# Optimization experiments

Hardware: AMD Instinct MI355X
Metric: run time of the kernel (lower is better)

Reference implementation:

```python
import jax, jax.numpy as jnp
import numpy as np

B, L, E, H = 4, 2048, 1024, 16
HD = E // H  # head_dim = 64


def setup_inputs() -> dict:
    key = jax.random.key(0)
    ks = jax.random.split(key, 11)
    s = 1.0 / np.sqrt(E)
    return {
        "q": jax.random.normal(ks[0], (B, L, E), jnp.float32),
        "k": jax.random.normal(ks[1], (B, L, E), jnp.float32),
        "v": jax.random.normal(ks[2], (B, L, E), jnp.float32),
        "Wq": jax.random.normal(ks[3], (E, E), jnp.float32) * s,
        "bq": jax.random.normal(ks[4], (E,), jnp.float32) * s,
        "Wk": jax.random.normal(ks[5], (E, E), jnp.float32) * s,
        "bk": jax.random.normal(ks[6], (E,), jnp.float32) * s,
        "Wv": jax.random.normal(ks[7], (E, E), jnp.float32) * s,
        "bv": jax.random.normal(ks[8], (E,), jnp.float32) * s,
        "Wo": jax.random.normal(ks[9], (E, E), jnp.float32) * s,
        "bo": jax.random.normal(ks[10], (E,), jnp.float32) * s,
    }


def reference(q, k, v, Wq, bq, Wk, bk, Wv, bv, Wo, bo):
    # Linear projections (torch Linear: x @ W.T + b)
    qp = q @ Wq.T + bq  # [B, L, E]
    kp = k @ Wk.T + bk
    vp = v @ Wv.T + bv
    # split heads -> [B, H, L, HD]
    qh = qp.reshape(B, L, H, HD).transpose(0, 2, 1, 3)
    kh = kp.reshape(B, L, H, HD).transpose(0, 2, 1, 3)
    vh = vp.reshape(B, L, H, HD).transpose(0, 2, 1, 3)
    scale = 1.0 / jnp.sqrt(jnp.asarray(HD, qh.dtype))
    score = jnp.einsum("bhqd,bhkd->bhqk", qh, kh) * scale  # [B, H, L, L]
    attn = jax.nn.softmax(score, axis=-1)
    # dropout p=0 (eval) -> identity
    out = jnp.einsum("bhqk,bhkd->bhqd", attn, vh)  # [B, H, L, HD]
    out = out.transpose(0, 2, 1, 3).reshape(B, L, E)
    out = out @ Wo.T + bo
    # original returns attn flattened over (B*H); match that shape
    return out, attn.reshape(B * H, L, L)
```

## Files before the change

kernel.cpp:

```cpp
#include <hip/hip_runtime.h>
#include <stdint.h>

typedef __attribute__((ext_vector_type(8))) short bf16x8;
typedef __attribute__((ext_vector_type(4))) float f32x4;

#define DEV __device__ __forceinline__

static constexpr int Bsz = 4, Lsz = 2048, Esz = 1024, Hsz = 16, HDsz = 64;
static constexpr int BL = Bsz * Lsz;
static constexpr size_t PLANE = (size_t)BL * Esz;

DEV unsigned short f2bf(float x) {
  union { float f; unsigned u; } c; c.f = x;
  unsigned u = c.u + 0x7FFFu + ((c.u >> 16) & 1u);
  return (unsigned short)(u >> 16);
}
DEV float bf2f(unsigned short h) {
  union { unsigned u; float f; } c; c.u = ((unsigned)h) << 16; return c.f;
}
DEV bf16x8 ld_bf8(const unsigned short* p) { return *(const bf16x8*)p; }

template<bool A_F32, bool OUT_F32>
DEV void gemm_body(const void* __restrict__ Aptr, const float* __restrict__ W,
                   const float* __restrict__ bias, void* __restrict__ Cptr,
                   unsigned short (*As)[40], unsigned short (*Bs)[40])
{
  constexpr int Kdim = Esz, Ndim = Esz;
  const int t = threadIdx.x;
  const int lane = t & 63, wave = t >> 6;
  const int wr = wave >> 1, wc = wave & 1;
  const int frow = lane & 15, fg = lane >> 4;

  const int f = blockIdx.x + 8 * blockIdx.y;
  const int m_t = ((f & 7) << 3) + (f >> 6);
  const int n_t = (f >> 3) & 7;
  const int m0 = m_t * 128, n0 = n_t * 128;

  f32x4 acc[4][4];
#pragma unroll
  for (int i = 0; i < 4; i++)
#pragma unroll
    for (int j = 0; j < 4; j++) acc[i][j] = f32x4{0.f, 0.f, 0.f, 0.f};

  for (int k0 = 0; k0 < Kdim; k0 += 32) {
    __syncthreads();
#pragma unroll
    for (int j = 0; j < 4; j++) {
      int s = t + j * 256, row = s >> 3, c4 = s & 7;
      if constexpr (A_F32) {
        const float* A = (const float*)Aptr;
        float4 v = *(const float4*)&A[(size_t)(m0 + row) * Kdim + k0 + c4 * 4];
        ushort4 hi;
        hi.x = f2bf(v.x); hi.y = f2bf(v.y); hi.z = f2bf(v.z); hi.w = f2bf(v.w);
        *(ushort4*)&As[row][c4 * 4] = hi;
      } else {
        const unsigned short* A = (const unsigned short*)Aptr;
        *(ushort4*)&As[row][c4 * 4] =
            *(const ushort4*)&A[(size_t)(m0 + row) * Kdim + k0 + c4 * 4];
      }
      {
        float4 v = *(const float4*)&W[(size_t)(n0 + row) * Kdim + k0 + c4 * 4];
        ushort4 hi;
        hi.x = f2bf(v.x); hi.y = f2bf(v.y); hi.z = f2bf(v.z); hi.w = f2bf(v.w);
        *(ushort4*)&Bs[row][c4 * 4] = hi;
      }
    }
    __syncthreads();

    bf16x8 ah[4], bhv[4];
#pragma unroll
    for (int x = 0; x < 4; x++) {
      ah[x] = ld_bf8(&As[wr * 64 + x * 16 + frow][fg * 8]);
      bhv[x] = ld_bf8(&Bs[wc * 64 + x * 16 + frow][fg * 8]);
    }
#pragma unroll
    for (int mi = 0; mi < 4; mi++)
#pragma unroll
      for (int ni = 0; ni < 4; ni++)
        acc[mi][ni] = __builtin_amdgcn_mfma_f32_16x16x32_bf16(ah[mi], bhv[ni], acc[mi][ni], 0, 0, 0);
  }

#pragma unroll
  for (int mi = 0; mi < 4; mi++)
#pragma unroll
    for (int ni = 0; ni < 4; ni++) {
      int col = n0 + wc * 64 + ni * 16 + frow;
      float bv = bias[col];
#pragma unroll
      for (int r = 0; r < 4; r++) {
        int row = m0 + wr * 64 + mi * 16 + fg * 4 + r;
        float val = acc[mi][ni][r] + bv;
        size_t idx = (size_t)row * Ndim + col;
        if constexpr (OUT_F32)
          __builtin_nontemporal_store(val, &((float*)Cptr)[idx]);
        else
          ((unsigned short*)Cptr)[idx] = f2bf(val);
      }
    }
}

__global__ __launch_bounds__(256) void gemm_proj3(
    const float* qA, const float* kA, const float* vA,
    const float* Wq, const float* Wk, const float* Wv,
    const float* bq, const float* bk, const float* bv,
    unsigned short* qC, unsigned short* kC, unsigned short* vC)
{
  __shared__ unsigned short As[128][40];
  __shared__ unsigned short Bs[128][40];
  const int z = blockIdx.z;
  const float* A = z == 0 ? qA : (z == 1 ? kA : vA);
  const float* W = z == 0 ? Wq : (z == 1 ? Wk : Wv);
  const float* bias = z == 0 ? bq : (z == 1 ? bk : bv);
  unsigned short* C = z == 0 ? qC : (z == 1 ? kC : vC);
  gemm_body<true, false>(A, W, bias, C, As, Bs);
}

__global__ __launch_bounds__(256) void gemm_out(
    const unsigned short* A, const float* W, const float* bias, float* C)
{
  __shared__ unsigned short As[128][40];
  __shared__ unsigned short Bs[128][40];
  gemm_body<false, true>(A, W, bias, C, As, Bs);
}

__global__ __launch_bounds__(256) void attn_fused(
    const unsigned short* __restrict__ qph, const unsigned short* __restrict__ kph,
    const unsigned short* __restrict__ vp,
    float* __restrict__ attn, unsigned short* __restrict__ oh)
{
  __shared__ unsigned short QP[64][72];
  __shared__ unsigned short Kh[64][72];
  __shared__ unsigned short Vt[64][72];

  const int t = threadIdx.x, lane = t & 63, wave = t >> 6;
  const int frow = lane & 15, fg = lane >> 4;

  const int f = blockIdx.x + 32 * blockIdx.y;
  const int bh = ((f & 7) << 3) + (f >> 8);
  const int qt = (f >> 3) & 31;
  const int b = bh >> 4, h = bh & 15;
  const int q0 = qt * 64;
  const int qw = q0 + wave * 16;

  const size_t base = (size_t)b * Lsz * Esz + (size_t)h * HDsz;
  constexpr float SC2 = 0.1803368801f;

  const int srow = t >> 4, sc4 = (t & 15) * 4;
  const int vrow = t >> 4, vc = t & 15;

  auto loadKh = [&](ushort4* r, int row0) {
#pragma unroll
    for (int j = 0; j < 4; j++)
      r[j] = *(const ushort4*)&kph[base + (size_t)(row0 + srow + j * 16) * Esz + sc4];
  };
  auto writeK = [&](unsigned short (*dst)[72], const ushort4* r) {
#pragma unroll
    for (int j = 0; j < 4; j++)
      *(ushort4*)&dst[srow + j * 16][sc4] = r[j];
  };
  auto loadV = [&](unsigned short (*rv)[4], int row0) {
#pragma unroll
    for (int j = 0; j < 4; j++) {
      size_t g = base + (size_t)(row0 + vrow + j * 16) * Esz + vc;
#pragma unroll
      for (int i = 0; i < 4; i++) rv[j][i] = vp[g + i * 16];
    }
  };
  auto writeV = [&](unsigned short (*rv)[4]) {
#pragma unroll
    for (int j = 0; j < 4; j++) {
#pragma unroll
      for (int i = 0; i < 4; i++) Vt[vc + i * 16][vrow + j * 16] = rv[j][i];
    }
  };

#pragma unroll
  for (int j = 0; j < 4; j++) {
    size_t g = base + (size_t)(q0 + srow + j * 16) * Esz + sc4;
    *(ushort4*)&QP[srow + j * 16][sc4] = *(const ushort4*)&qph[g];
  }
  __syncthreads();
  bf16x8 qfh[2];
#pragma unroll
  for (int dh = 0; dh < 2; dh++)
    qfh[dh] = ld_bf8(&QP[wave * 16 + frow][dh * 32 + fg * 8]);

  float zl[4];
#pragma unroll
  for (int r = 0; r < 4; r++) zl[r] = 0.f;

  auto computeA = [&](unsigned short (*Kc)[72]) {
#pragma unroll
    for (int kc = 0; kc < 4; kc++) {
      f32x4 sv = f32x4{0.f, 0.f, 0.f, 0.f};
#pragma unroll
      for (int dh = 0; dh < 2; dh++) {
        bf16x8 kf = ld_bf8(&Kc[kc * 16 + frow][dh * 32 + fg * 8]);
        sv = __builtin_amdgcn_mfma_f32_16x16x32_bf16(qfh[dh], kf, sv, 0, 0, 0);
      }
#pragma unroll
      for (int r = 0; r < 4; r++) zl[r] += exp2f(sv[r] * SC2);
    }
  };

  {
    ushort4 rA[4], rB[4];
    loadKh(rA, 0);
    loadKh(rB, 64);
    for (int kt = 0; kt < 32; kt += 2) {
      __syncthreads();
      writeK(Kh, rA);
      writeK(Vt, rB);
      if (kt + 2 < 32) {
        loadKh(rA, (kt + 2) * 64);
        loadKh(rB, (kt + 3) * 64);
      }
      __syncthreads();
      computeA(Kh);
      computeA(Vt);
    }
  }
  float rz[4];
#pragma unroll
  for (int r = 0; r < 4; r++) {
    float z = zl[r];
#pragma unroll
    for (int o = 1; o < 16; o <<= 1) z += __shfl_xor(z, o);
    rz[r] = 1.f / z;
  }

  f32x4 oacc[4];
#pragma unroll
  for (int d = 0; d < 4; d++) oacc[d] = f32x4{0.f, 0.f, 0.f, 0.f};

  const size_t arow = (size_t)bh * Lsz * Lsz;

  auto computeB = [&](int kt) {
    f32x4 sv[4];
#pragma unroll
    for (int kc = 0; kc < 4; kc++) {
      sv[kc] = f32x4{0.f, 0.f, 0.f, 0.f};
#pragma unroll
      for (int dh = 0; dh < 2; dh++) {
        bf16x8 kfh = ld_bf8(&Kh[kc * 16 + frow][dh * 32 + fg * 8]);
        sv[kc] = __builtin_amdgcn_mfma_f32_16x16x32_bf16(qfh[dh], kfh, sv[kc], 0, 0, 0);
      }
    }
#pragma unroll
    for (int kc = 0; kc < 4; kc++) {
#pragma unroll
      for (int r = 0; r < 4; r++) {
        float p = exp2f(sv[kc][r] * SC2) * rz[r];
        QP[wave * 16 + fg * 4 + r][kc * 16 + frow] = f2bf(p);
      }
    }
    __syncthreads();
#pragma unroll
    for (int it = 0; it < 4; it++) {
      int prow = it * 4 + fg;
      int pc = frow * 4;
      ushort4 pv4 = *(const ushort4*)&QP[wave * 16 + prow][pc];
      f32x4 w;
      w[0] = bf2f(pv4.x); w[1] = bf2f(pv4.y); w[2] = bf2f(pv4.z); w[3] = bf2f(pv4.w);
      __builtin_nontemporal_store(w,
          (f32x4*)&attn[arow + (size_t)(qw + prow) * Lsz + kt * 64 + pc]);
    }
#pragma unroll
    for (int kh2 = 0; kh2 < 2; kh2++) {
      bf16x8 pa = ld_bf8(&QP[wave * 16 + frow][kh2 * 32 + fg * 8]);
#pragma unroll
      for (int d = 0; d < 4; d++) {
        bf16x8 vb = ld_bf8(&Vt[d * 16 + frow][kh2 * 32 + fg * 8]);
        oacc[d] = __builtin_amdgcn_mfma_f32_16x16x32_bf16(pa, vb, oacc[d], 0, 0, 0);
      }
    }
  };

  {
    ushort4 khA[4], khB[4];
    unsigned short vA[4][4], vB[4][4];
    loadKh(khA, 0);
    loadV(vA, 0);
    for (int kt = 0; kt < 32; kt += 2) {
      __syncthreads();
      writeK(Kh, khA);
      writeV(vA);
      if (kt + 1 < 32) {
        loadKh(khB, (kt + 1) * 64);
        loadV(vB, (kt + 1) * 64);
      }
      __syncthreads();
      computeB(kt);
      __syncthreads();
      writeK(Kh, khB);
      writeV(vB);
      if (kt + 2 < 32) {
        loadKh(khA, (kt + 2) * 64);
        loadV(vA, (kt + 2) * 64);
      }
      __syncthreads();
      computeB(kt + 1);
    }
  }

#pragma unroll
  for (int d = 0; d < 4; d++)
#pragma unroll
    for (int r = 0; r < 4; r++) {
      int qrow = qw + fg * 4 + r;
      __builtin_nontemporal_store(f2bf(oacc[d][r]),
          &oh[base + (size_t)qrow * Esz + d * 16 + frow]);
    }
}

extern "C" void kernel_launch(void* const* d_in, const int* in_sizes, int n_in,
                              void* d_out, int out_size, void* d_ws, size_t ws_size,
                              hipStream_t stream)
{
  (void)in_sizes; (void)n_in; (void)out_size; (void)ws_size;

  const float* q  = (const float*)d_in[0];
  const float* k  = (const float*)d_in[1];
  const float* v  = (const float*)d_in[2];
  const float* Wq = (const float*)d_in[3];
  const float* bq = (const float*)d_in[4];
  const float* Wk = (const float*)d_in[5];
  const float* bk = (const float*)d_in[6];
  const float* Wv = (const float*)d_in[7];
  const float* bv = (const float*)d_in[8];
  const float* Wo = (const float*)d_in[9];
  const float* bo = (const float*)d_in[10];

  float* out  = (float*)d_out;
  float* attn = out + PLANE;

  unsigned short* qph = (unsigned short*)d_ws;
  unsigned short* kph = qph + PLANE;
  unsigned short* vpp = kph + PLANE;
  unsigned short* oh  = vpp + PLANE;

  dim3 bb(256);
  gemm_proj3<<<dim3(8, 64, 3), bb, 0, stream>>>(q, k, v, Wq, Wk, Wv,
                                                bq, bk, bv, qph, kph, vpp);

  dim3 ga(32, 64);
  attn_fused<<<ga, bb, 0, stream>>>(qph, kph, vpp, attn, oh);

  gemm_out<<<dim3(8, 64), bb, 0, stream>>>(oh, Wo, bo, out);
}
```

Baseline: 463.5 us.

## Move softmax denominator pass into separate kernel with larger 128x128 tiles

The first pass of the two-pass softmax, which sums exp of the scores per row, moves out of the fused attention kernel into a new zcalc kernel. zcalc uses 128-row Q tiles against 128-row K tiles so each K load is reused over twice as many query rows. It writes the reciprocal row sums to workspace, and attn_fused reads them instead of recomputing. A __syncthreads between writing P to shared memory and reading it back is also dropped. That removal looks safe only because each wave touches just its own 16 rows of QP, so it is a correctness risk if that ever changes.

```diff
diff --git a/kernel.cpp b/kernel.cpp
--- a/kernel.cpp
+++ b/kernel.cpp
@@ -123,9 +123,104 @@
   gemm_body<false, true>(A, W, bias, C, As, Bs);
 }
 
+__global__ __launch_bounds__(256) void zcalc(
+    const unsigned short* __restrict__ qph, const unsigned short* __restrict__ kph,
+    float* __restrict__ rzg)
+{
+  __shared__ unsigned short Qs[128][72];
+  __shared__ unsigned short Ks[128][72];
+
+  const int t = threadIdx.x, lane = t & 63, wave = t >> 6;
+  const int frow = lane & 15, fg = lane >> 4;
+
+  const int f = blockIdx.x + 16 * blockIdx.y;
+  const int bh = ((f & 7) << 3) + (f >> 7);
+  const int qt = (f >> 3) & 15;
+  const int b = bh >> 4, h = bh & 15;
+  const int q0 = qt * 128;
+  const size_t base = (size_t)b * Lsz * Esz + (size_t)h * HDsz;
+  constexpr float SC2 = 0.1803368801f;
+
+  const int srow = t >> 4, sc4 = (t & 15) * 4;
+
+  auto load128 = [&](ushort4* r, const unsigned short* src, int row0) {
+#pragma unroll
+    for (int j = 0; j < 8; j++)
+      r[j] = *(const ushort4*)&src[base + (size_t)(row0 + srow + j * 16) * Esz + sc4];
+  };
+  auto write128 = [&](unsigned short (*dst)[72], const ushort4* r) {
+#pragma unroll
+    for (int j = 0; j < 8; j++)
+      *(ushort4*)&dst[srow + j * 16][sc4] = r[j];
+  };
+
+  {
+    ushort4 rq[8];
+    load128(rq, qph, q0);
+    write128(Qs, rq);
+  }
+  __syncthreads();
+  bf16x8 qf[2][2];
+#pragma unroll
+  for (int mi = 0; mi < 2; mi++)
+#pragma unroll
+    for (int dh = 0; dh < 2; dh++)
+      qf[mi][dh] = ld_bf8(&Qs[wave * 32 + mi * 16 + frow][dh * 32 + fg * 8]);
+
+  float zl[2][4];
+#pragma unroll
+  for (int mi = 0; mi < 2; mi++)
+#pragma unroll
+    for (int r = 0; r < 4; r++) zl[mi][r] = 0.f;
+
+  auto compute = [&]() {
+#pragma unroll
+    for (int kf = 0; kf < 8; kf++) {
+      bf16x8 k0 = ld_bf8(&Ks[kf * 16 + frow][fg * 8]);
+      bf16x8 k1 = ld_bf8(&Ks[kf * 16 + frow][32 + fg * 8]);
+#pragma unroll
+      for (int mi = 0; mi < 2; mi++) {
+        f32x4 sv = f32x4{0.f, 0.f, 0.f, 0.f};
+        sv = __builtin_amdgcn_mfma_f32_16x16x32_bf16(qf[mi][0], k0, sv, 0, 0, 0);
+        sv = __builtin_amdgcn_mfma_f32_16x16x32_bf16(qf[mi][1], k1, sv, 0, 0, 0);
+#pragma unroll
+        for (int r = 0; r < 4; r++) zl[mi][r] += exp2f(sv[r] * SC2);
+      }
+    }
+  };
+
+  {
+    ushort4 rA[8], rB[8];
+    load128(rA, kph, 0);
+    for (int kt = 0; kt < 16; kt += 2) {
+      __syncthreads();
+      write128(Ks, rA);
+      if (kt + 1 < 16) load128(rB, kph, (kt + 1) * 128);
+      __syncthreads();
+      compute();
+      __syncthreads();
+      write128(Ks, rB);
+      if (kt + 2 < 16) load128(rA, kph, (kt + 2) * 128);
+      __syncthreads();
+      compute();
+    }
+  }
+
+#pragma unroll
+  for (int mi = 0; mi < 2; mi++)
+#pragma unroll
+    for (int r = 0; r < 4; r++) {
+      float z = zl[mi][r];
+#pragma unroll
+      for (int o = 1; o < 16; o <<= 1) z += __shfl_xor(z, o);
+      if (frow == 0)
+        rzg[(size_t)bh * Lsz + q0 + wave * 32 + mi * 16 + fg * 4 + r] = 1.f / z;
+    }
+}
+
 __global__ __launch_bounds__(256) void attn_fused(
     const unsigned short* __restrict__ qph, const unsigned short* __restrict__ kph,
-    const unsigned short* __restrict__ vp,
+    const unsigned short* __restrict__ vp, const float* __restrict__ rzg,
     float* __restrict__ attn, unsigned short* __restrict__ oh)
 {
   __shared__ unsigned short QP[64][72];
@@ -185,49 +280,10 @@
   for (int dh = 0; dh < 2; dh++)
     qfh[dh] = ld_bf8(&QP[wave * 16 + frow][dh * 32 + fg * 8]);
 
-  float zl[4];
-#pragma unroll
-  for (int r = 0; r < 4; r++) zl[r] = 0.f;
-
-  auto computeA = [&](unsigned short (*Kc)[72]) {
-#pragma unroll
-    for (int kc = 0; kc < 4; kc++) {
-      f32x4 sv = f32x4{0.f, 0.f, 0.f, 0.f};
-#pragma unroll
-      for (int dh = 0; dh < 2; dh++) {
-        bf16x8 kf = ld_bf8(&Kc[kc * 16 + frow][dh * 32 + fg * 8]);
-        sv = __builtin_amdgcn_mfma_f32_16x16x32_bf16(qfh[dh], kf, sv, 0, 0, 0);
-      }
-#pragma unroll
-      for (int r = 0; r < 4; r++) zl[r] += exp2f(sv[r] * SC2);
-    }
-  };
-
-  {
-    ushort4 rA[4], rB[4];
-    loadKh(rA, 0);
-    loadKh(rB, 64);
-    for (int kt = 0; kt < 32; kt += 2) {
-      __syncthreads();
-      writeK(Kh, rA);
-      writeK(Vt, rB);
-      if (kt + 2 < 32) {
-        loadKh(rA, (kt + 2) * 64);
-        loadKh(rB, (kt + 3) * 64);
-      }
-      __syncthreads();
-      computeA(Kh);
-      computeA(Vt);
-    }
-  }
   float rz[4];
 #pragma unroll
-  for (int r = 0; r < 4; r++) {
-    float z = zl[r];
-#pragma unroll
-    for (int o = 1; o < 16; o <<= 1) z += __shfl_xor(z, o);
-    rz[r] = 1.f / z;
-  }
+  for (int r = 0; r < 4; r++)
+    rz[r] = rzg[(size_t)bh * Lsz + qw + fg * 4 + r];
 
   f32x4 oacc[4];
 #pragma unroll
@@ -254,7 +310,6 @@
         QP[wave * 16 + fg * 4 + r][kc * 16 + frow] = f2bf(p);
       }
     }
-    __syncthreads();
 #pragma unroll
     for (int it = 0; it < 4; it++) {
       int prow = it * 4 + fg;
@@ -338,13 +393,16 @@
   unsigned short* kph = qph + PLANE;
   unsigned short* vpp = kph + PLANE;
   unsigned short* oh  = vpp + PLANE;
+  float* rzg = (float*)(oh + PLANE);
 
   dim3 bb(256);
   gemm_proj3<<<dim3(8, 64, 3), bb, 0, stream>>>(q, k, v, Wq, Wk, Wv,
                                                 bq, bk, bv, qph, kph, vpp);
 
+  zcalc<<<dim3(16, 64), bb, 0, stream>>>(qph, kph, rzg);
+
   dim3 ga(32, 64);
-  attn_fused<<<ga, bb, 0, stream>>>(qph, kph, vpp, attn, oh);
+  attn_fused<<<ga, bb, 0, stream>>>(qph, kph, vpp, rzg, attn, oh);
 
   gemm_out<<<dim3(8, 64), bb, 0, stream>>>(oh, Wo, bo, out);
 }
```

Result: no change. 460.8 us (-0.6%).
